# Optimization experiments

Hardware: AMD Instinct MI355X
Metric: run time of the kernel (lower is better)

## Reference

```python
import jax, jax.numpy as jnp
import numpy as np

GROUPS = 32
EPS = 1e-5
S = 8  # cluster grid side


def group_norm(y, gamma, beta):
    B, C, H, W = y.shape
    yg = y.reshape(B, GROUPS, C // GROUPS, H, W)
    m = yg.mean(axis=(2, 3, 4), keepdims=True)
    v = yg.var(axis=(2, 3, 4), keepdims=True)
    yn = ((yg - m) * jax.lax.rsqrt(v + EPS)).reshape(B, C, H, W)
    return yn * gamma[:, None, None] + beta[:, None, None]


def setup_inputs() -> dict:
    key = jax.random.key(0)
    ks = jax.random.split(key, 6)
    B, C, H, W = 8, 256, 128, 128
    K = S * S  # 64 clusters
    x = jax.random.normal(ks[0], (B, C, H, W), dtype=jnp.float32)
    centers = jax.random.normal(ks[1], (K, C), dtype=jnp.float32) * 0.02
    dw_w = jax.random.normal(ks[2], (C, 1, 7, 7), dtype=jnp.float32) * 0.05  # depthwise 7x7
    dw_b = jax.random.normal(ks[3], (C,), dtype=jnp.float32) * 0.02
    pw_w = jax.random.normal(ks[4], (C, C), dtype=jnp.float32) * 0.02       # 1x1 conv
    pw_b = jax.random.normal(ks[5], (C,), dtype=jnp.float32) * 0.02
    gn_g = jnp.ones((C,), dtype=jnp.float32)
    gn_b = jnp.zeros((C,), dtype=jnp.float32)
    return {"x": x, "centers": centers, "dw_w": dw_w, "dw_b": dw_b,
            "pw_w": pw_w, "pw_b": pw_b, "gn_g": gn_g, "gn_b": gn_b}


def reference(x, centers, dw_w, dw_b, pw_w, pw_b, gn_g, gn_b):
    B, C, H, W = x.shape
    x_flat = x.reshape(B, C, H * W).transpose(0, 2, 1)            # [B,N,C]
    sim = jnp.einsum('bnc,kc->bnk', x_flat, centers) * (C ** -0.5)
    attn = jax.nn.softmax(sim, axis=-1)                            # [B,N,K]
    cluster = jnp.einsum('bnk,bnc->bkc', attn, x_flat)             # attn^T @ x
    grid = cluster.transpose(0, 2, 1).reshape(B, C, S, S)          # [B,C,8,8]
    refined = jax.lax.conv_general_dilated(
        grid, dw_w, window_strides=(1, 1), padding=((3, 3), (3, 3)),
        feature_group_count=C,
        dimension_numbers=('NCHW', 'OIHW', 'NCHW')) + dw_b[:, None, None]
    refined = jax.nn.silu(refined)
    refined_flat = refined.reshape(B, C, S * S).transpose(0, 2, 1)  # [B,K,C]
    out = jnp.einsum('bnk,bkc->bnc', attn, refined_flat)            # unpool
    out = out.transpose(0, 2, 1).reshape(B, C, H, W)
    y = jnp.einsum('bchw,oc->bohw', out, pw_w) + pw_b[:, None, None]
    return x + group_norm(y, gn_g, gn_b)
```

## Files before the change

### kernel.cpp

```cpp
#include <hip/hip_runtime.h>
#include <math.h>

#define BB 8
#define CCH 256
#define NN 16384
#define KK 64
#define SEGS 64

typedef __attribute__((ext_vector_type(8))) short bf16x8;
typedef __attribute__((ext_vector_type(4))) float f32x4;
#define MFMA16 __builtin_amdgcn_mfma_f32_16x16x32_bf16

constexpr size_t OFF_ATTN = 0;
constexpr size_t OFF_CTT  = 4194304;
constexpr size_t OFF_PWT  = 4210688;
constexpr size_t OFF_GT   = 4276224;
constexpr size_t OFF_CLUP = 4341760;
constexpr size_t OFF_MP   = 8536064;
constexpr size_t OFF_ABP  = 9584640;
constexpr size_t OFF_CLUS = 9617408;
constexpr size_t OFF_MS2  = 9748480;
constexpr size_t OFF_ABS2 = 9781248;
constexpr size_t OFF_QP   = 9781760;
constexpr size_t OFF_REF  = OFF_CLUP;
constexpr size_t OFF_G    = OFF_CLUP + 131072;
constexpr size_t OFF_MU   = OFF_CLUP + 262144;
constexpr size_t OFF_RS   = OFF_CLUP + 262400;

__device__ __forceinline__ unsigned short f2bf(float f) {
    unsigned int x = __float_as_uint(f);
    unsigned int r = (x + 0x7FFFu + ((x >> 16) & 1u)) >> 16;
    return (unsigned short)r;
}
__device__ __forceinline__ float bf2f(unsigned short u) {
    return __uint_as_float(((unsigned int)u) << 16);
}

__global__ __launch_bounds__(256) void p0_prep(const float* __restrict__ centers,
                                               const float* __restrict__ pw_w,
                                               float* __restrict__ ws) {
    int idx = blockIdx.x * 256 + threadIdx.x;
    if (idx < 16384)
        ((unsigned short*)(ws + OFF_CTT))[idx] = f2bf(centers[idx] * 0.0625f);
    int c = idx >> 8, o = idx & 255;
    ws[OFF_PWT + idx] = pw_w[o * CCH + c];
}

__global__ __launch_bounds__(256, 2) void p1_attn(const float* __restrict__ x,
                                                  float* __restrict__ ws) {
    __shared__ __align__(16) unsigned char smem[59392];
    unsigned short* xTh = (unsigned short*)(smem + 32768);
    float*          S   = (float*)(smem + 32768);
    unsigned short* aT  = (unsigned short*)(smem + 50176);
    float*          scr = (float*)(smem + 50176);

    const int tid = threadIdx.x;
    const int w  = tid >> 6;
    const int l  = tid & 63;
    const int lr = l & 15;
    const int lg = l >> 4;
    const int b   = blockIdx.y;
    const int seg = blockIdx.x;
    const int cstage = tid >> 4;
    const int n4     = tid & 15;

    const unsigned short* ctb = (const unsigned short*)(ws + OFF_CTT);
    unsigned short* attn_bf = (unsigned short*)(ws + OFF_ATTN);

    bf16x8 bc[8];
#pragma unroll
    for (int cs = 0; cs < 8; ++cs)
        bc[cs] = *(const bf16x8*)(ctb + (w * 16 + lr) * CCH + cs * 32 + lg * 8);

    f32x4 cacc[4][4] = {};
    f32x4 macc[4]    = {};
    float ab_acc = 0.f;

    float4 v[8];
    {
#pragma unroll
        for (int it = 0; it < 8; ++it) {
            int c = it * 16 + cstage;
            v[it] = *(const float4*)&x[((size_t)(b * CCH + c)) * NN + seg * 256 + 4 * n4];
        }
    }

#pragma unroll 1
    for (int sub = 0; sub < 4; ++sub) {
        const int ns0 = seg * 256 + sub * 64;
        f32x4 sacc[4] = {};

#pragma unroll
        for (int h = 0; h < 2; ++h) {
            __syncthreads();
#pragma unroll
            for (int it = 0; it < 8; ++it) {
                int c = h * 128 + it * 16 + cstage;
                int cl = c & 127;
                ushort4 bv;
                bv.x = f2bf(v[it].x); bv.y = f2bf(v[it].y);
                bv.z = f2bf(v[it].z); bv.w = f2bf(v[it].w);
                *(ushort4*)(smem + ((c * 128 + 8 * n4) ^ ((c & 7) << 4))) = bv;
                xTh[(4 * n4 + 0) * 136 + cl] = bv.x;
                xTh[(4 * n4 + 1) * 136 + cl] = bv.y;
                xTh[(4 * n4 + 2) * 136 + cl] = bv.z;
                xTh[(4 * n4 + 3) * 136 + cl] = bv.w;
            }
            if (!(sub == 3 && h == 1)) {
                const int nsub = sub + h;
                const int nh = h ^ 1;
                const int pns0 = seg * 256 + nsub * 64;
#pragma unroll
                for (int it = 0; it < 8; ++it) {
                    int c = nh * 128 + it * 16 + cstage;
                    v[it] = *(const float4*)&x[((size_t)(b * CCH + c)) * NN + pns0 + 4 * n4];
                }
            }
            __syncthreads();
#pragma unroll
            for (int cc = 0; cc < 4; ++cc) {
                const int co = cc * 32 + lg * 8;
                bf16x8 a0 = *(const bf16x8*)(xTh + (lr     ) * 136 + co);
                bf16x8 a1 = *(const bf16x8*)(xTh + (16 + lr) * 136 + co);
                bf16x8 a2 = *(const bf16x8*)(xTh + (32 + lr) * 136 + co);
                bf16x8 a3 = *(const bf16x8*)(xTh + (48 + lr) * 136 + co);
                bf16x8 bfr = bc[h * 4 + cc];
                sacc[0] = MFMA16(a0, bfr, sacc[0], 0, 0, 0);
                sacc[1] = MFMA16(a1, bfr, sacc[1], 0, 0, 0);
                sacc[2] = MFMA16(a2, bfr, sacc[2], 0, 0, 0);
                sacc[3] = MFMA16(a3, bfr, sacc[3], 0, 0, 0);
            }
        }
        __syncthreads();
#pragma unroll
        for (int nt = 0; nt < 4; ++nt)
#pragma unroll
            for (int r = 0; r < 4; ++r)
                S[(nt * 16 + lg * 4 + r) * 68 + w * 16 + lr] = sacc[nt][r];
        __syncthreads();

        {
            const int rn = tid >> 2, q = tid & 3;
            float e[16];
#pragma unroll
            for (int m = 0; m < 4; ++m) {
                float4 vv = *(float4*)&S[rn * 68 + q * 16 + 4 * m];
                e[4*m+0] = vv.x; e[4*m+1] = vv.y; e[4*m+2] = vv.z; e[4*m+3] = vv.w;
            }
            float mx = -1e30f;
#pragma unroll
            for (int t = 0; t < 16; ++t) mx = fmaxf(mx, e[t]);
            mx = fmaxf(mx, __shfl_xor(mx, 1, 64));
            mx = fmaxf(mx, __shfl_xor(mx, 2, 64));
            float ls = 0.f;
#pragma unroll
            for (int t = 0; t < 16; ++t) { e[t] = __expf(e[t] - mx); ls += e[t]; }
            ls += __shfl_xor(ls, 1, 64);
            ls += __shfl_xor(ls, 2, 64);
            float rinv = 1.f / ls;
            unsigned short bt16[16];
#pragma unroll
            for (int t = 0; t < 16; ++t) {
                bt16[t] = f2bf(e[t] * rinv);
                aT[(q * 16 + t) * 72 + rn] = bt16[t];
            }
            unsigned int* gdst = (unsigned int*)(attn_bf + ((size_t)b * NN + ns0 + rn) * KK + q * 16);
            uint4 pk0, pk1;
            pk0.x = (unsigned int)bt16[0]  | ((unsigned int)bt16[1]  << 16);
            pk0.y = (unsigned int)bt16[2]  | ((unsigned int)bt16[3]  << 16);
            pk0.z = (unsigned int)bt16[4]  | ((unsigned int)bt16[5]  << 16);
            pk0.w = (unsigned int)bt16[6]  | ((unsigned int)bt16[7]  << 16);
            pk1.x = (unsigned int)bt16[8]  | ((unsigned int)bt16[9]  << 16);
            pk1.y = (unsigned int)bt16[10] | ((unsigned int)bt16[11] << 16);
            pk1.z = (unsigned int)bt16[12] | ((unsigned int)bt16[13] << 16);
            pk1.w = (unsigned int)bt16[14] | ((unsigned int)bt16[15] << 16);
            *(uint4*)gdst = pk0;
            *(uint4*)(gdst + 4) = pk1;
        }
        __syncthreads();

        {
            const int kk = tid & 63;
#pragma unroll
            for (int m = 0; m < 4; ++m) {
                ushort4 av = *(const ushort4*)(aT + kk * 72 + w * 16 + 4 * m);
                ab_acc += bf2f(av.x) + bf2f(av.y) + bf2f(av.z) + bf2f(av.w);
            }
        }
#pragma unroll
        for (int s = 0; s < 2; ++s) {
            const int no = s * 32 + lg * 8;
            bf16x8 am = *(const bf16x8*)(aT + (w * 16 + lr) * 72 + no);
#pragma unroll
            for (int k1t = 0; k1t < 4; ++k1t) {
                bf16x8 bm = *(const bf16x8*)(aT + (k1t * 16 + lr) * 72 + no);
                macc[k1t] = MFMA16(am, bm, macc[k1t], 0, 0, 0);
            }
        }
#pragma unroll
        for (int s = 0; s < 2; ++s) {
            const int no = s * 32 + lg * 8;
            bf16x8 aa0 = *(const bf16x8*)(aT + (lr     ) * 72 + no);
            bf16x8 aa1 = *(const bf16x8*)(aT + (16 + lr) * 72 + no);
            bf16x8 aa2 = *(const bf16x8*)(aT + (32 + lr) * 72 + no);
            bf16x8 aa3 = *(const bf16x8*)(aT + (48 + lr) * 72 + no);
#pragma unroll
            for (int ct = 0; ct < 4; ++ct) {
                const int c = w * 64 + ct * 16 + lr;
                bf16x8 bb = *(const bf16x8*)(smem + ((c * 128 + no * 2) ^ ((c & 7) << 4)));
                cacc[0][ct] = MFMA16(aa0, bb, cacc[0][ct], 0, 0, 0);
                cacc[1][ct] = MFMA16(aa1, bb, cacc[1][ct], 0, 0, 0);
                cacc[2][ct] = MFMA16(aa2, bb, cacc[2][ct], 0, 0, 0);
                cacc[3][ct] = MFMA16(aa3, bb, cacc[3][ct], 0, 0, 0);
            }
        }
    }

    __syncthreads();
    {
        unsigned short* stg = (unsigned short*)smem;
#pragma unroll
        for (int kt = 0; kt < 4; ++kt)
#pragma unroll
            for (int ct = 0; ct < 4; ++ct) {
                const int c = w * 64 + ct * 16 + lr;
#pragma unroll
                for (int r = 0; r < 4; ++r) {
                    const int row = kt * 16 + lg * 4 + r;
                    stg[row * 256 + (c ^ ((row & 7) << 3))] = f2bf(cacc[kt][ct][r]);
                }
            }
    }
#pragma unroll
    for (int k1t = 0; k1t < 4; ++k1t)
#pragma unroll
        for (int r = 0; r < 4; ++r)
            S[(w * 16 + lg * 4 + r) * 68 + k1t * 16 + lr] = macc[k1t][r];
    scr[(tid & 63) * 4 + (tid >> 6)] = ab_acc;
    __syncthreads();
    {
        uint4* gb = (uint4*)((unsigned short*)(ws + OFF_CLUP) + (size_t)(seg * BB + b) * 16384);
        const uint4* s4 = (const uint4*)smem;
#pragma unroll
        for (int it = 0; it < 8; ++it) {
            int f = it * 256 + tid;
            gb[f] = s4[(f >> 5) * 32 + ((f & 31) ^ ((f >> 5) & 7))];
        }
    }
    {
        unsigned int* mp32 = (unsigned int*)((unsigned short*)(ws + OFF_MP) + (size_t)(seg * BB + b) * 4096);
#pragma unroll
        for (int it = 0; it < 8; ++it) {
            int flat = it * 256 + tid;
            int k2 = flat >> 5, kp = flat & 31;
            unsigned int pv = (unsigned int)f2bf(S[k2 * 68 + 2 * kp])
                            | ((unsigned int)f2bf(S[k2 * 68 + 2 * kp + 1]) << 16);
            mp32[flat] = pv;
        }
    }
    if (tid < 64)
        ws[OFF_ABP + (size_t)(seg * BB + b) * KK + tid] =
            scr[tid * 4 + 0] + scr[tid * 4 + 1] + scr[tid * 4 + 2] + scr[tid * 4 + 3];
}

__global__ __launch_bounds__(256) void p15_reduce(float* __restrict__ ws) {
    const int blk = blockIdx.x;
    if (blk < 512) {
        const int b = blk >> 6, k = blk & 63, c = threadIdx.x;
        const unsigned short* clu_p = (const unsigned short*)(ws + OFF_CLUP);
        float s = 0.f;
#pragma unroll 8
        for (int seg = 0; seg < SEGS; ++seg)
            s += bf2f(clu_p[((size_t)((seg * BB + b) * KK + k)) * CCH + c]);
        ws[OFF_CLUS + ((size_t)(b * KK + k)) * CCH + c] = s;
    } else {
        const int t = blk - 512;
        const int b = t >> 3, part = t & 7;
        const unsigned short* m_p = (const unsigned short*)(ws + OFF_MP);
#pragma unroll
        for (int it = 0; it < 2; ++it) {
            int idx = part * 512 + it * 256 + threadIdx.x;
            float s = 0.f;
#pragma unroll 8
            for (int seg = 0; seg < SEGS; ++seg)
                s += bf2f(m_p[(size_t)(seg * BB + b) * 4096 + idx]);
            ws[OFF_MS2 + (size_t)b * 4096 + idx] = s;
        }
        if (part == 0 && threadIdx.x < 64) {
            float s = 0.f;
#pragma unroll 8
            for (int seg = 0; seg < SEGS; ++seg)
                s += ws[OFF_ABP + (size_t)(seg * BB + b) * KK + threadIdx.x];
            ws[OFF_ABS2 + b * KK + threadIdx.x] = s;
        }
    }
}

__global__ __launch_bounds__(256) void p2_dw(const float* __restrict__ dw_w,
                                             const float* __restrict__ dw_b,
                                             float* __restrict__ ws) {
    __shared__ float clu_s[64][256];
    const int b = blockIdx.y;
    const int kq = blockIdx.x;
    const int tid = threadIdx.x;
    float* ref = ws + OFF_REF;

    for (int k = 0; k < 64; ++k)
        clu_s[k][tid] = ws[OFF_CLUS + ((size_t)(b * KK + k)) * CCH + tid];
    float w[49];
#pragma unroll
    for (int t = 0; t < 49; ++t) w[t] = dw_w[tid * 49 + t];
    float bias = dw_b[tid];
    __syncthreads();

    for (int it = 0; it < 16; ++it) {
        int k = kq * 16 + it;
        int ky = k >> 3, kx = k & 7;
        float v = 0.f;
#pragma unroll
        for (int dy = 0; dy < 7; ++dy) {
            int yy = ky + dy - 3;
            if (yy < 0 || yy > 7) continue;
#pragma unroll
            for (int dx = 0; dx < 7; ++dx) {
                int xx = kx + dx - 3;
                if (xx < 0 || xx > 7) continue;
                v += clu_s[yy * 8 + xx][tid] * w[dy * 7 + dx];
            }
        }
        v += bias;
        float sv = v / (1.f + expf(-v));
        ref[((size_t)b * KK + k) * CCH + tid] = sv;
    }
}

__global__ __launch_bounds__(256) void p2_g(const float* __restrict__ pw_b,
                                            float* __restrict__ ws) {
    __shared__ float rs[256];
    const int b = blockIdx.y, k = blockIdx.x, tid = threadIdx.x;
    const float* ref = ws + OFF_REF;
    const float* pwT = ws + OFF_PWT;
    float* G = ws + OFF_G;
    rs[tid] = ref[((size_t)b * KK + k) * CCH + tid];
    __syncthreads();
    float g = pw_b[tid];
#pragma unroll 8
    for (int c = 0; c < 256; ++c)
        g += rs[c] * pwT[c * CCH + tid];
    G[((size_t)b * KK + k) * CCH + tid] = g;
    ((unsigned short*)(ws + OFF_GT))[((size_t)b * CCH + tid) * KK + k] = f2bf(g);
}

__global__ __launch_bounds__(256) void p2_w(float* __restrict__ ws) {
    __shared__ float Mrows[512];
    const int kq = blockIdx.x, b = blockIdx.y;
    const int tid = threadIdx.x;
#pragma unroll
    for (int it = 0; it < 2; ++it) {
        int idx = it * 256 + tid;
        Mrows[idx] = ws[OFF_MS2 + (size_t)b * 4096 + kq * 512 + idx] * (1.0f / 16384.0f);
    }
    __syncthreads();
    const float* G = ws + OFF_G + (size_t)b * KK * CCH;
    float t0 = 0.f, t1 = 0.f, t2 = 0.f, t3 = 0.f;
    float t4 = 0.f, t5 = 0.f, t6 = 0.f, t7 = 0.f;
#pragma unroll 8
    for (int k2 = 0; k2 < 64; ++k2) {
        float g = G[k2 * CCH + tid];
        t0 += Mrows[0 * 64 + k2] * g;
        t1 += Mrows[1 * 64 + k2] * g;
        t2 += Mrows[2 * 64 + k2] * g;
        t3 += Mrows[3 * 64 + k2] * g;
        t4 += Mrows[4 * 64 + k2] * g;
        t5 += Mrows[5 * 64 + k2] * g;
        t6 += Mrows[6 * 64 + k2] * g;
        t7 += Mrows[7 * 64 + k2] * g;
    }
    const float* Gk = G + (size_t)(kq * 8) * CCH + tid;
    float qp = t0 * Gk[0 * CCH] + t1 * Gk[1 * CCH] + t2 * Gk[2 * CCH] + t3 * Gk[3 * CCH]
             + t4 * Gk[4 * CCH] + t5 * Gk[5 * CCH] + t6 * Gk[6 * CCH] + t7 * Gk[7 * CCH];
    ws[OFF_QP + (size_t)(b * 8 + kq) * CCH + tid] = qp;
}

__global__ __launch_bounds__(256) void p2_stats(float* __restrict__ ws) {
    __shared__ float abs_[64];
    __shared__ float mu_s[256];
    __shared__ float q_s[256];
    const int b = blockIdx.x, tid = threadIdx.x;
    if (tid < 64)
        abs_[tid] = ws[OFF_ABS2 + b * KK + tid] * (1.0f / 16384.0f);
    __syncthreads();

    const float* G = ws + OFF_G + (size_t)b * KK * CCH;
    float mu = 0.f;
#pragma unroll 8
    for (int k = 0; k < 64; ++k)
        mu += abs_[k] * G[(size_t)k * CCH + tid];
    const float* qp = ws + OFF_QP + (size_t)b * 8 * CCH + tid;
    float q = 0.f;
#pragma unroll
    for (int kq = 0; kq < 8; ++kq)
        q += qp[(size_t)kq * CCH];
    mu_s[tid] = mu;
    q_s[tid] = q;
    __syncthreads();
    if (tid < 32) {
        float m = 0.f, e = 0.f;
#pragma unroll
        for (int j = 0; j < 8; ++j) { m += mu_s[tid * 8 + j]; e += q_s[tid * 8 + j]; }
        m *= 0.125f; e *= 0.125f;
        float var = e - m * m;
        ws[OFF_MU + b * 32 + tid] = m;
        ws[OFF_RS + b * 32 + tid] = rsqrtf(fmaxf(var, 0.f) + 1e-5f);
    }
}

__global__ __launch_bounds__(256, 3) void p3_out(const float* __restrict__ x,
                                                 const float* __restrict__ gamma,
                                                 const float* __restrict__ beta,
                                                 const float* __restrict__ ws,
                                                 float* __restrict__ out) {
    __shared__ __align__(16) unsigned char sm3[8192];
    const int tid = threadIdx.x;
    const int w  = tid >> 6;
    const int l  = tid & 63;
    const int lr = l & 15;
    const int lg = l >> 4;
    const int n0 = blockIdx.x * 64;
    const int b  = blockIdx.y;

    const unsigned short* attn_bf = (const unsigned short*)(ws + OFF_ATTN);
    const unsigned short* GTb = (const unsigned short*)(ws + OFF_GT) + (size_t)b * CCH * KK;

    bf16x8 bg0[4], bg1[4];
#pragma unroll
    for (int ot = 0; ot < 4; ++ot) {
        const int o = w * 64 + ot * 16 + lr;
        bg0[ot] = *(const bf16x8*)(GTb + (size_t)o * KK + 0 * 32 + lg * 8);
        bg1[ot] = *(const bf16x8*)(GTb + (size_t)o * KK + 1 * 32 + lg * 8);
    }

    {
        const uint4* asrc = (const uint4*)(attn_bf + ((size_t)b * NN + n0) * KK);
#pragma unroll
        for (int it = 0; it < 2; ++it) {
            int flat = it * 256 + tid;
            int n = flat >> 3, c16 = flat & 7;
            *(uint4*)(sm3 + ((n * 128 + c16 * 16) ^ ((n & 7) << 4))) = asrc[n * 8 + c16];
        }
    }
    __syncthreads();

    f32x4 acc[4][4] = {};
#pragma unroll
    for (int kh = 0; kh < 2; ++kh) {
        bf16x8 af[4];
#pragma unroll
        for (int nt = 0; nt < 4; ++nt) {
            int n = nt * 16 + lr;
            af[nt] = *(const bf16x8*)(sm3 + ((n * 128 + (kh * 64 + lg * 16)) ^ ((n & 7) << 4)));
        }
#pragma unroll
        for (int nt = 0; nt < 4; ++nt)
#pragma unroll
            for (int ot = 0; ot < 4; ++ot)
                acc[nt][ot] = MFMA16(af[nt], kh ? bg1[ot] : bg0[ot], acc[nt][ot], 0, 0, 0);
    }

#pragma unroll
    for (int ot = 0; ot < 4; ++ot) {
        const int o = w * 64 + ot * 16 + lr;
        const int grp = o >> 3;
        const float m = ws[OFF_MU + b * 32 + grp];
        const float r = ws[OFF_RS + b * 32 + grp];
        const float gm = gamma[o] * r;
        const float bt = beta[o];
#pragma unroll
        for (int nt = 0; nt < 4; ++nt) {
            const int n = n0 + nt * 16 + lg * 4;
            size_t base = ((size_t)(b * CCH + o)) * NN + n;
            float4 xv = *(const float4*)&x[base];
            f32x4 a = acc[nt][ot];
            float4 ov;
            ov.x = xv.x + (a[0] - m) * gm + bt;
            ov.y = xv.y + (a[1] - m) * gm + bt;
            ov.z = xv.z + (a[2] - m) * gm + bt;
            ov.w = xv.w + (a[3] - m) * gm + bt;
            *(float4*)&out[base] = ov;
        }
    }
}

extern "C" void kernel_launch(void* const* d_in, const int* in_sizes, int n_in,
                              void* d_out, int out_size, void* d_ws, size_t ws_size,
                              hipStream_t stream) {
    (void)in_sizes; (void)n_in; (void)out_size; (void)ws_size;
    const float* x       = (const float*)d_in[0];
    const float* centers = (const float*)d_in[1];
    const float* dw_w    = (const float*)d_in[2];
    const float* dw_b    = (const float*)d_in[3];
    const float* pw_w    = (const float*)d_in[4];
    const float* pw_b    = (const float*)d_in[5];
    const float* gn_g    = (const float*)d_in[6];
    const float* gn_b    = (const float*)d_in[7];
    float* out = (float*)d_out;
    float* ws  = (float*)d_ws;

    p0_prep<<<256, 256, 0, stream>>>(centers, pw_w, ws);
    p1_attn<<<dim3(64, 8), 256, 0, stream>>>(x, ws);
    p15_reduce<<<576, 256, 0, stream>>>(ws);
    p2_dw<<<dim3(4, 8), 256, 0, stream>>>(dw_w, dw_b, ws);
    p2_g<<<dim3(64, 8), 256, 0, stream>>>(pw_b, ws);
    p2_w<<<dim3(8, 8), 256, 0, stream>>>(ws);
    p2_stats<<<8, 256, 0, stream>>>(ws);
    p3_out<<<dim3(256, 8), 256, 0, stream>>>(x, gn_g, gn_b, ws, out);
}
```

Before: 347.7 us.

## Compute softmax directly from MFMA accumulators by swapping operand roles

The similarity MFMA is restructured so each wave owns 16 pixel columns and all 64 clusters, with centers as the A operand read straight from global memory each iteration instead of held in registers. Softmax is then done in registers with cross-lane shuffles, which removes the fp32 S staging buffer in shared memory and two block barriers. The cost is repeated global or cache loads of the center tile inside the inner loop and a strided shared-memory read to pack the attention rows for the global write.

```diff
diff --git a/kernel.cpp b/kernel.cpp
--- a/kernel.cpp
+++ b/kernel.cpp
@@ -67,11 +67,6 @@
     const unsigned short* ctb = (const unsigned short*)(ws + OFF_CTT);
     unsigned short* attn_bf = (unsigned short*)(ws + OFF_ATTN);
 
-    bf16x8 bc[8];
-#pragma unroll
-    for (int cs = 0; cs < 8; ++cs)
-        bc[cs] = *(const bf16x8*)(ctb + (w * 16 + lr) * CCH + cs * 32 + lg * 8);
-
     f32x4 cacc[4][4] = {};
     f32x4 macc[4]    = {};
     float ab_acc = 0.f;
@@ -120,64 +115,67 @@
 #pragma unroll
             for (int cc = 0; cc < 4; ++cc) {
                 const int co = cc * 32 + lg * 8;
-                bf16x8 a0 = *(const bf16x8*)(xTh + (lr     ) * 136 + co);
-                bf16x8 a1 = *(const bf16x8*)(xTh + (16 + lr) * 136 + co);
-                bf16x8 a2 = *(const bf16x8*)(xTh + (32 + lr) * 136 + co);
-                bf16x8 a3 = *(const bf16x8*)(xTh + (48 + lr) * 136 + co);
-                bf16x8 bfr = bc[h * 4 + cc];
-                sacc[0] = MFMA16(a0, bfr, sacc[0], 0, 0, 0);
-                sacc[1] = MFMA16(a1, bfr, sacc[1], 0, 0, 0);
-                sacc[2] = MFMA16(a2, bfr, sacc[2], 0, 0, 0);
-                sacc[3] = MFMA16(a3, bfr, sacc[3], 0, 0, 0);
-            }
-        }
-        __syncthreads();
-#pragma unroll
-        for (int nt = 0; nt < 4; ++nt)
-#pragma unroll
-            for (int r = 0; r < 4; ++r)
-                S[(nt * 16 + lg * 4 + r) * 68 + w * 16 + lr] = sacc[nt][r];
+                bf16x8 bx = *(const bf16x8*)(xTh + (w * 16 + lr) * 136 + co);
+                const unsigned short* cbase = ctb + (h * 4 + cc) * 32 + lg * 8;
+                bf16x8 c0 = *(const bf16x8*)(cbase + (size_t)(0 * 16 + lr) * CCH);
+                bf16x8 c1 = *(const bf16x8*)(cbase + (size_t)(1 * 16 + lr) * CCH);
+                bf16x8 c2 = *(const bf16x8*)(cbase + (size_t)(2 * 16 + lr) * CCH);
+                bf16x8 c3 = *(const bf16x8*)(cbase + (size_t)(3 * 16 + lr) * CCH);
+                sacc[0] = MFMA16(c0, bx, sacc[0], 0, 0, 0);
+                sacc[1] = MFMA16(c1, bx, sacc[1], 0, 0, 0);
+                sacc[2] = MFMA16(c2, bx, sacc[2], 0, 0, 0);
+                sacc[3] = MFMA16(c3, bx, sacc[3], 0, 0, 0);
+            }
+        }
+
+        {
+            float mx = -1e30f;
+#pragma unroll
+            for (int kt = 0; kt < 4; ++kt)
+#pragma unroll
+                for (int r = 0; r < 4; ++r) mx = fmaxf(mx, sacc[kt][r]);
+            mx = fmaxf(mx, __shfl_xor(mx, 16, 64));
+            mx = fmaxf(mx, __shfl_xor(mx, 32, 64));
+            f32x4 e[4];
+            float ls = 0.f;
+#pragma unroll
+            for (int kt = 0; kt < 4; ++kt)
+#pragma unroll
+                for (int r = 0; r < 4; ++r) {
+                    float ev = __expf(sacc[kt][r] - mx);
+                    e[kt][r] = ev;
+                    ls += ev;
+                }
+            ls += __shfl_xor(ls, 16, 64);
+            ls += __shfl_xor(ls, 32, 64);
+            float rinv = 1.f / ls;
+#pragma unroll
+            for (int kt = 0; kt < 4; ++kt)
+#pragma unroll
+                for (int r = 0; r < 4; ++r)
+                    aT[(kt * 16 + lg * 4 + r) * 72 + w * 16 + lr] = f2bf(e[kt][r] * rinv);
+        }
         __syncthreads();
 
         {
             const int rn = tid >> 2, q = tid & 3;
-            float e[16];
-#pragma unroll
-            for (int m = 0; m < 4; ++m) {
-                float4 vv = *(float4*)&S[rn * 68 + q * 16 + 4 * m];
-                e[4*m+0] = vv.x; e[4*m+1] = vv.y; e[4*m+2] = vv.z; e[4*m+3] = vv.w;
-            }
-            float mx = -1e30f;
-#pragma unroll
-            for (int t = 0; t < 16; ++t) mx = fmaxf(mx, e[t]);
-            mx = fmaxf(mx, __shfl_xor(mx, 1, 64));
-            mx = fmaxf(mx, __shfl_xor(mx, 2, 64));
-            float ls = 0.f;
-#pragma unroll
-            for (int t = 0; t < 16; ++t) { e[t] = __expf(e[t] - mx); ls += e[t]; }
-            ls += __shfl_xor(ls, 1, 64);
-            ls += __shfl_xor(ls, 2, 64);
-            float rinv = 1.f / ls;
-            unsigned short bt16[16];
-#pragma unroll
-            for (int t = 0; t < 16; ++t) {
-                bt16[t] = f2bf(e[t] * rinv);
-                aT[(q * 16 + t) * 72 + rn] = bt16[t];
-            }
+            unsigned short t16[16];
+#pragma unroll
+            for (int j = 0; j < 16; ++j)
+                t16[j] = aT[(q * 16 + j) * 72 + rn];
+            uint4 pk0, pk1;
+            pk0.x = (unsigned int)t16[0]  | ((unsigned int)t16[1]  << 16);
+            pk0.y = (unsigned int)t16[2]  | ((unsigned int)t16[3]  << 16);
+            pk0.z = (unsigned int)t16[4]  | ((unsigned int)t16[5]  << 16);
+            pk0.w = (unsigned int)t16[6]  | ((unsigned int)t16[7]  << 16);
+            pk1.x = (unsigned int)t16[8]  | ((unsigned int)t16[9]  << 16);
+            pk1.y = (unsigned int)t16[10] | ((unsigned int)t16[11] << 16);
+            pk1.z = (unsigned int)t16[12] | ((unsigned int)t16[13] << 16);
+            pk1.w = (unsigned int)t16[14] | ((unsigned int)t16[15] << 16);
             unsigned int* gdst = (unsigned int*)(attn_bf + ((size_t)b * NN + ns0 + rn) * KK + q * 16);
-            uint4 pk0, pk1;
-            pk0.x = (unsigned int)bt16[0]  | ((unsigned int)bt16[1]  << 16);
-            pk0.y = (unsigned int)bt16[2]  | ((unsigned int)bt16[3]  << 16);
-            pk0.z = (unsigned int)bt16[4]  | ((unsigned int)bt16[5]  << 16);
-            pk0.w = (unsigned int)bt16[6]  | ((unsigned int)bt16[7]  << 16);
-            pk1.x = (unsigned int)bt16[8]  | ((unsigned int)bt16[9]  << 16);
-            pk1.y = (unsigned int)bt16[10] | ((unsigned int)bt16[11] << 16);
-            pk1.z = (unsigned int)bt16[12] | ((unsigned int)bt16[13] << 16);
-            pk1.w = (unsigned int)bt16[14] | ((unsigned int)bt16[15] << 16);
             *(uint4*)gdst = pk0;
             *(uint4*)(gdst + 4) = pk1;
         }
-        __syncthreads();
 
         {
             const int kk = tid & 63;
```

Result: slower. 375.2 us (+7.9%).
